# Kernel optimization log

Measured on AMD Instinct MI355X. Metric: run time of the kernel, lower is better.

The kernel has to match this reference:

```python
import jax, jax.numpy as jnp
import numpy as np

N_NODES = 100000
N_FEAT = 256
N_EDGES = 3200000
N_CLUSTERS = 16
COLLAPSE_REG = 0.1


def setup_inputs() -> dict:
    key = jax.random.key(0)
    k1, k2, k3, k4 = jax.random.split(key, 4)
    features = jax.random.normal(k1, (N_NODES, N_FEAT), dtype=jnp.float32)
    edge_row = jax.random.randint(k2, (N_EDGES,), 0, N_NODES, dtype=jnp.int32)
    edge_col = jax.random.randint(k3, (N_EDGES,), 0, N_NODES, dtype=jnp.int32)
    edge_val = jnp.ones((N_EDGES,), dtype=jnp.float32)
    # orthogonal-ish init approximated by scaled normal (init does not affect math)
    W = jax.random.normal(k4, (N_FEAT, N_CLUSTERS), dtype=jnp.float32) / np.float32(np.sqrt(N_FEAT))
    b = jnp.zeros((N_CLUSTERS,), dtype=jnp.float32)
    return {"features": features, "W": W, "b": b,
            "edge_row": edge_row, "edge_col": edge_col, "edge_val": edge_val}


def reference(features, W, b, edge_row, edge_col, edge_val):
    n = features.shape[0]
    k = W.shape[1]
    # assignment softmax (dropout_rate=0 -> identity)
    assignments = jax.nn.softmax(features @ W + b, axis=1)  # [n, k]
    cluster_sizes = assignments.sum(axis=0)                  # [k]
    assignments_pooling = assignments / cluster_sizes        # [n, k]
    # degrees = sparse row sums of adjacency
    degrees = jax.ops.segment_sum(edge_val, edge_row, num_segments=n)[:, None]  # [n, 1]
    n_edges = degrees.sum() / 2
    # sparse mm: adjacency @ assignments via gather + segment_sum
    adj_assign = jax.ops.segment_sum(edge_val[:, None] * assignments[edge_col],
                                     edge_row, num_segments=n)  # [n, k]
    graph_pooled = assignments.T @ adj_assign                # [k, k]
    normalizer_left = assignments.T @ degrees                # [k, 1]
    normalizer_right = degrees.T @ assignments               # [1, k]
    normalizer = normalizer_left @ normalizer_right / (2 * n_edges)
    spectral_loss = -jnp.trace(graph_pooled - normalizer) / (2 * n_edges)
    collapse_loss = COLLAPSE_REG * (jnp.linalg.norm(cluster_sizes) / n
                                    * jnp.sqrt(jnp.float32(k)) - 1.0)
    features_pooled = jax.nn.selu(assignments_pooling.T @ features)  # [k, d]
    return features_pooled, assignments, spectral_loss, collapse_loss
```

## Files before the change

kernel.cpp:

```cpp
#include <hip/hip_runtime.h>
#include <math.h>

#define KC 16
#define DF 256

#define WS_POOLED 0
#define WS_CS     4096
#define WS_M      4112
#define WS_TR     4128
#define WS_ESUM   4129
#define WS_TOTAL  4130
#define S8_OFF_BYTES 16640

typedef float v2f  __attribute__((ext_vector_type(2)));
typedef unsigned int u32x4 __attribute__((ext_vector_type(4)));

__global__ void zero_ws_kernel(float* __restrict__ ws) {
  int i = blockIdx.x * blockDim.x + threadIdx.x;
  if (i < WS_TOTAL) ws[i] = 0.0f;
}

__device__ __forceinline__ unsigned pk4_fp8(float a, float b, float c, float d) {
  unsigned w = (unsigned)__builtin_amdgcn_cvt_pk_fp8_f32(a, b, 0, false);
  w = (unsigned)__builtin_amdgcn_cvt_pk_fp8_f32(c, d, (int)w, true);
  return w;
}
__device__ __forceinline__ void cvt4_fp8(unsigned w, float* f) {
  v2f p = __builtin_amdgcn_cvt_pk_f32_fp8(w, false);
  f[0] = p.x; f[1] = p.y;
  p = __builtin_amdgcn_cvt_pk_f32_fp8(w, true);
  f[2] = p.x; f[3] = p.y;
}
__device__ __forceinline__ void cvt16_fp8(u32x4 u, float* f) {
  cvt4_fp8(u.x, f); cvt4_fp8(u.y, f + 4);
  cvt4_fp8(u.z, f + 8); cvt4_fp8(u.w, f + 12);
}

__global__ void __launch_bounds__(256) assign_kernel(
    const float* __restrict__ F, const float* __restrict__ W,
    const float* __restrict__ b, float* __restrict__ S,
    unsigned* __restrict__ S8, float* __restrict__ ws, int n) {
  __shared__ float Ft[32 * 257];
  __shared__ float cs_l[KC];
  const int t = threadIdx.x;
  if (t < KC) cs_l[t] = 0.0f;
  const int nb = blockIdx.x << 8;
  const int node = nb + t;
  const bool valid = node < n;
  const bool interior = (nb + 256 <= n);

  const int nl = t >> 3;
  const int jc = t & 7;

  float4 pref[8];
  auto load_chunk = [&](int s) {
    #pragma unroll
    for (int it = 0; it < 8; ++it) {
      const int nn = nl + (it << 5);
      if (interior || nb + nn < n)
        pref[it] = *(const float4*)&F[(size_t)(nb + nn) * DF + (s << 5) + (jc << 2)];
      else
        pref[it] = make_float4(0.f, 0.f, 0.f, 0.f);
    }
  };

  float acc[KC];
  #pragma unroll
  for (int k = 0; k < KC; ++k) acc[k] = 0.f;

  load_chunk(0);
  for (int s = 0; s < 8; ++s) {
    __syncthreads();
    #pragma unroll
    for (int it = 0; it < 8; ++it) {
      const int nn = nl + (it << 5);
      const int d0 = jc << 2;
      Ft[(d0 + 0) * 257 + nn] = pref[it].x;
      Ft[(d0 + 1) * 257 + nn] = pref[it].y;
      Ft[(d0 + 2) * 257 + nn] = pref[it].z;
      Ft[(d0 + 3) * 257 + nn] = pref[it].w;
    }
    __syncthreads();
    if (s < 7) load_chunk(s + 1);
    #pragma unroll
    for (int j = 0; j < 8; ++j) {
      const float fv0 = Ft[(4 * j + 0) * 257 + t];
      const float fv1 = Ft[(4 * j + 1) * 257 + t];
      const float fv2 = Ft[(4 * j + 2) * 257 + t];
      const float fv3 = Ft[(4 * j + 3) * 257 + t];
      const float* __restrict__ Wg = &W[(size_t)((s << 5) + (j << 2)) * KC];
      #pragma unroll
      for (int k = 0; k < KC; ++k)
        acc[k] += fv0 * Wg[k] + fv1 * Wg[KC + k]
                + fv2 * Wg[2 * KC + k] + fv3 * Wg[3 * KC + k];
    }
  }

  float mx = -1e30f;
  #pragma unroll
  for (int k = 0; k < KC; ++k) { acc[k] += b[k]; mx = fmaxf(mx, acc[k]); }
  float sum = 0.f;
  #pragma unroll
  for (int k = 0; k < KC; ++k) { acc[k] = __expf(acc[k] - mx); sum += acc[k]; }
  const float inv = 1.0f / sum;
  #pragma unroll
  for (int k = 0; k < KC; ++k) acc[k] *= inv;
  if (!valid) {
    #pragma unroll
    for (int k = 0; k < KC; ++k) acc[k] = 0.f;
  }
  if (valid) {
    float4* __restrict__ So = (float4*)&S[(size_t)node * KC];
    So[0] = make_float4(acc[0],  acc[1],  acc[2],  acc[3]);
    So[1] = make_float4(acc[4],  acc[5],  acc[6],  acc[7]);
    So[2] = make_float4(acc[8],  acc[9],  acc[10], acc[11]);
    So[3] = make_float4(acc[12], acc[13], acc[14], acc[15]);
    if (S8) {
      u32x4 p;
      p.x = pk4_fp8(acc[0],  acc[1],  acc[2],  acc[3]);
      p.y = pk4_fp8(acc[4],  acc[5],  acc[6],  acc[7]);
      p.z = pk4_fp8(acc[8],  acc[9],  acc[10], acc[11]);
      p.w = pk4_fp8(acc[12], acc[13], acc[14], acc[15]);
      *(u32x4*)&S8[(size_t)node * 4] = p;
    }
  }
  #pragma unroll
  for (int off = 1; off < 64; off <<= 1) {
    #pragma unroll
    for (int k = 0; k < KC; ++k) acc[k] += __shfl_xor(acc[k], off);
  }
  if ((t & 63) == 0) {
    #pragma unroll
    for (int k = 0; k < KC; ++k) atomicAdd(&cs_l[k], acc[k]);
  }
  __syncthreads();
  if (t < KC) atomicAdd(&ws[WS_CS + t], cs_l[t]);
}

__device__ __forceinline__ void acc_edge8(u32x4 ar, u32x4 ac, float v,
                                          float* m, float& tr, float& es) {
  float a[16], bb[16];
  cvt16_fp8(ar, a);
  cvt16_fp8(ac, bb);
  float d = 0.f;
  #pragma unroll
  for (int k = 0; k < 16; ++k) d += a[k] * bb[k];
  tr += v * d;
  es += v;
  #pragma unroll
  for (int k = 0; k < 16; ++k) m[k] += v * a[k];
}

__global__ void __launch_bounds__(256) edge_kernel_fp8(
    const int* __restrict__ erow, const int* __restrict__ ecol,
    const float* __restrict__ evl, const u32x4* __restrict__ S8,
    float* __restrict__ ws, int ne) {
  __shared__ float red[KC + 2];
  const int t = threadIdx.x;
  if (t < KC + 2) red[t] = 0.0f;
  __syncthreads();

  float m[KC];
  #pragma unroll
  for (int i = 0; i < KC; ++i) m[i] = 0.f;
  float tr = 0.f, es = 0.f;

  const int tid = blockIdx.x * 256 + t;
  const int stride = gridDim.x * 256;
  for (int e0 = tid; e0 < ne; e0 += 4 * stride) {
    const int eB = e0 + stride, eC = e0 + 2 * stride, eD = e0 + 3 * stride;
    int rA = __builtin_nontemporal_load(&erow[e0]);
    int cA = __builtin_nontemporal_load(&ecol[e0]);
    float vA = __builtin_nontemporal_load(&evl[e0]);
    int rB = 0, cB = 0, rC = 0, cC = 0, rD = 0, cD = 0;
    float vB = 0.f, vC = 0.f, vD = 0.f;
    if (eB < ne) { rB = __builtin_nontemporal_load(&erow[eB]);
                   cB = __builtin_nontemporal_load(&ecol[eB]);
                   vB = __builtin_nontemporal_load(&evl[eB]); }
    if (eC < ne) { rC = __builtin_nontemporal_load(&erow[eC]);
                   cC = __builtin_nontemporal_load(&ecol[eC]);
                   vC = __builtin_nontemporal_load(&evl[eC]); }
    if (eD < ne) { rD = __builtin_nontemporal_load(&erow[eD]);
                   cD = __builtin_nontemporal_load(&ecol[eD]);
                   vD = __builtin_nontemporal_load(&evl[eD]); }
    const u32x4 aA = __builtin_nontemporal_load(&S8[rA]);
    const u32x4 bA = __builtin_nontemporal_load(&S8[cA]);
    const u32x4 aB = __builtin_nontemporal_load(&S8[rB]);
    const u32x4 bB = __builtin_nontemporal_load(&S8[cB]);
    const u32x4 aC = __builtin_nontemporal_load(&S8[rC]);
    const u32x4 bC = __builtin_nontemporal_load(&S8[cC]);
    const u32x4 aD = __builtin_nontemporal_load(&S8[rD]);
    const u32x4 bD = __builtin_nontemporal_load(&S8[cD]);
    acc_edge8(aA, bA, vA, m, tr, es);
    acc_edge8(aB, bB, vB, m, tr, es);
    acc_edge8(aC, bC, vC, m, tr, es);
    acc_edge8(aD, bD, vD, m, tr, es);
  }
  #pragma unroll
  for (int off = 1; off < 64; off <<= 1) {
    tr += __shfl_xor(tr, off);
    es += __shfl_xor(es, off);
    #pragma unroll
    for (int i = 0; i < KC; ++i) m[i] += __shfl_xor(m[i], off);
  }
  if ((t & 63) == 0) {
    atomicAdd(&red[KC], tr);
    atomicAdd(&red[KC + 1], es);
    #pragma unroll
    for (int i = 0; i < KC; ++i) atomicAdd(&red[i], m[i]);
  }
  __syncthreads();
  if (t < KC)            atomicAdd(&ws[WS_M + t], red[t]);
  else if (t == KC)      atomicAdd(&ws[WS_TR], red[KC]);
  else if (t == KC + 1)  atomicAdd(&ws[WS_ESUM], red[KC + 1]);
}

__global__ void __launch_bounds__(256) edge_kernel_f32(
    const int* __restrict__ erow, const int* __restrict__ ecol,
    const float* __restrict__ evl, const float* __restrict__ S,
    float* __restrict__ ws, int ne) {
  __shared__ float red[KC + 2];
  const int t = threadIdx.x;
  if (t < KC + 2) red[t] = 0.0f;
  __syncthreads();
  float m[KC];
  #pragma unroll
  for (int i = 0; i < KC; ++i) m[i] = 0.f;
  float tr = 0.f, es = 0.f;
  const int stride = gridDim.x * blockDim.x;
  for (int e = blockIdx.x * blockDim.x + t; e < ne; e += stride) {
    const int r = erow[e];
    const int c = ecol[e];
    const float v = evl[e];
    const float4* __restrict__ Sr = (const float4*)(S + (size_t)r * KC);
    const float4* __restrict__ Sc = (const float4*)(S + (size_t)c * KC);
    const float4 a0 = Sr[0], a1 = Sr[1], a2 = Sr[2], a3 = Sr[3];
    const float4 b0 = Sc[0], b1 = Sc[1], b2 = Sc[2], b3 = Sc[3];
    float d = a0.x*b0.x + a0.y*b0.y + a0.z*b0.z + a0.w*b0.w
            + a1.x*b1.x + a1.y*b1.y + a1.z*b1.z + a1.w*b1.w
            + a2.x*b2.x + a2.y*b2.y + a2.z*b2.z + a2.w*b2.w
            + a3.x*b3.x + a3.y*b3.y + a3.z*b3.z + a3.w*b3.w;
    tr += v * d; es += v;
    m[0]+=v*a0.x; m[1]+=v*a0.y; m[2]+=v*a0.z; m[3]+=v*a0.w;
    m[4]+=v*a1.x; m[5]+=v*a1.y; m[6]+=v*a1.z; m[7]+=v*a1.w;
    m[8]+=v*a2.x; m[9]+=v*a2.y; m[10]+=v*a2.z; m[11]+=v*a2.w;
    m[12]+=v*a3.x; m[13]+=v*a3.y; m[14]+=v*a3.z; m[15]+=v*a3.w;
  }
  #pragma unroll
  for (int off = 1; off < 64; off <<= 1) {
    tr += __shfl_xor(tr, off);
    es += __shfl_xor(es, off);
    #pragma unroll
    for (int i = 0; i < KC; ++i) m[i] += __shfl_xor(m[i], off);
  }
  if ((t & 63) == 0) {
    atomicAdd(&red[KC], tr);
    atomicAdd(&red[KC + 1], es);
    #pragma unroll
    for (int i = 0; i < KC; ++i) atomicAdd(&red[i], m[i]);
  }
  __syncthreads();
  if (t < KC)            atomicAdd(&ws[WS_M + t], red[t]);
  else if (t == KC)      atomicAdd(&ws[WS_TR], red[KC]);
  else if (t == KC + 1)  atomicAdd(&ws[WS_ESUM], red[KC + 1]);
}

__global__ void __launch_bounds__(256) pool_kernel(
    const float* __restrict__ F, const float* __restrict__ S,
    float* __restrict__ ws, int n) {
  const int t = threadIdx.x;
  float acc[KC];
  #pragma unroll
  for (int i = 0; i < KC; ++i) acc[i] = 0.f;

  const int nch = n >> 5;
  for (int ch = blockIdx.x; ch < nch; ch += gridDim.x) {
    const int base = ch << 5;
    float fl[32];
    #pragma unroll
    for (int i = 0; i < 32; ++i)
      fl[i] = F[(size_t)(base + i) * DF + t];
    #pragma unroll
    for (int i = 0; i < 32; ++i) {
      const float4* __restrict__ Sr = (const float4*)(S + (size_t)(base + i) * KC);
      const float4 s0 = Sr[0], s1 = Sr[1], s2 = Sr[2], s3 = Sr[3];
      const float f = fl[i];
      acc[0]+=f*s0.x;  acc[1]+=f*s0.y;  acc[2]+=f*s0.z;  acc[3]+=f*s0.w;
      acc[4]+=f*s1.x;  acc[5]+=f*s1.y;  acc[6]+=f*s1.z;  acc[7]+=f*s1.w;
      acc[8]+=f*s2.x;  acc[9]+=f*s2.y;  acc[10]+=f*s2.z; acc[11]+=f*s2.w;
      acc[12]+=f*s3.x; acc[13]+=f*s3.y; acc[14]+=f*s3.z; acc[15]+=f*s3.w;
    }
  }
  if (blockIdx.x == 0) {
    for (int i2 = nch << 5; i2 < n; ++i2) {
      const float f = F[(size_t)i2 * DF + t];
      const float* __restrict__ Sr = S + (size_t)i2 * KC;
      #pragma unroll
      for (int kk = 0; kk < KC; ++kk) acc[kk] += f * Sr[kk];
    }
  }
  #pragma unroll
  for (int kk = 0; kk < KC; ++kk)
    atomicAdd(&ws[WS_POOLED + kk * DF + t], acc[kk]);
}

__global__ void finalize_kernel(const float* __restrict__ ws,
                                float* __restrict__ out, int n) {
  const int t = threadIdx.x;
  const float alpha = 1.6732632423543772f;
  const float scale = 1.0507009873554805f;
  for (int idx = t; idx < KC * DF; idx += blockDim.x) {
    const int k = idx >> 8;
    const float x = ws[WS_POOLED + idx] / ws[WS_CS + k];
    const float r = x > 0.f ? x : alpha * expm1f(x);
    out[idx] = scale * r;
  }
  if (t == 0) {
    const float esum = ws[WS_ESUM];
    const float tr = ws[WS_TR];
    float sm2 = 0.f, sc2 = 0.f;
    for (int i = 0; i < KC; ++i) {
      const float mi = ws[WS_M + i];
      sm2 += mi * mi;
      const float ci = ws[WS_CS + i];
      sc2 += ci * ci;
    }
    const float spectral = -(tr - sm2 / esum) / esum;
    const float collapse = 0.1f * (sqrtf(sc2) / (float)n * 4.0f - 1.0f);
    const size_t off = (size_t)(KC * DF) + (size_t)n * KC;
    out[off] = spectral;
    out[off + 1] = collapse;
  }
}

extern "C" void kernel_launch(void* const* d_in, const int* in_sizes, int n_in,
                              void* d_out, int out_size, void* d_ws, size_t ws_size,
                              hipStream_t stream) {
  const float* F   = (const float*)d_in[0];
  const float* W   = (const float*)d_in[1];
  const float* b   = (const float*)d_in[2];
  const int* erow  = (const int*)d_in[3];
  const int* ecol  = (const int*)d_in[4];
  const float* evl = (const float*)d_in[5];
  const int n  = in_sizes[0] / DF;
  const int ne = in_sizes[3];
  float* out = (float*)d_out;
  float* S   = out + KC * DF;
  float* ws  = (float*)d_ws;

  const bool use_fp8 = ws_size >= (size_t)S8_OFF_BYTES + (size_t)n * 16 + 64;
  unsigned* S8 = use_fp8 ? (unsigned*)((char*)d_ws + S8_OFF_BYTES) : nullptr;

  zero_ws_kernel<<<(WS_TOTAL + 255) / 256, 256, 0, stream>>>(ws);
  assign_kernel<<<(n + 255) / 256, 256, 0, stream>>>(F, W, b, S, S8, ws, n);
  if (use_fp8)
    edge_kernel_fp8<<<2048, 256, 0, stream>>>(erow, ecol, evl, (const u32x4*)S8, ws, ne);
  else
    edge_kernel_f32<<<2048, 256, 0, stream>>>(erow, ecol, evl, S, ws, ne);
  pool_kernel<<<1024, 256, 0, stream>>>(F, S, ws, n);
  finalize_kernel<<<1, 256, 0, stream>>>(ws, out, n);
}
```

Baseline: 340.8 us.

## Bin edges into 4096x4096 node tiles and process each tile from LDS

```diff
diff --git a/kernel.cpp b/kernel.cpp
--- a/kernel.cpp
+++ b/kernel.cpp
@@ -10,14 +10,20 @@
 #define WS_TR     4128
 #define WS_ESUM   4129
 #define WS_TOTAL  4130
-#define S8_OFF_BYTES 16640
+#define S8_OFF_BYTES  16640
+#define CUR_OFF_BYTES 2097152
+#define REC_OFF_BYTES 4194304
+#define MAXNB 1024
 
 typedef float v2f  __attribute__((ext_vector_type(2)));
 typedef unsigned int u32x4 __attribute__((ext_vector_type(4)));
-
-__global__ void zero_ws_kernel(float* __restrict__ ws) {
+typedef unsigned int u32x2 __attribute__((ext_vector_type(2)));
+
+__global__ void zero_ws_kernel(float* __restrict__ ws, unsigned* __restrict__ cur,
+                               int nb) {
   int i = blockIdx.x * blockDim.x + threadIdx.x;
   if (i < WS_TOTAL) ws[i] = 0.0f;
+  if (cur && i < nb) cur[i] = 0u;
 }
 
 __device__ __forceinline__ unsigned pk4_fp8(float a, float b, float c, float d) {
@@ -34,6 +40,19 @@
 __device__ __forceinline__ void cvt16_fp8(u32x4 u, float* f) {
   cvt4_fp8(u.x, f); cvt4_fp8(u.y, f + 4);
   cvt4_fp8(u.z, f + 8); cvt4_fp8(u.w, f + 12);
+}
+__device__ __forceinline__ void acc_edge8(u32x4 ar, u32x4 ac, float v,
+                                          float* m, float& tr, float& es) {
+  float a[16], bb[16];
+  cvt16_fp8(ar, a);
+  cvt16_fp8(ac, bb);
+  float d = 0.f;
+  #pragma unroll
+  for (int k = 0; k < 16; ++k) d += a[k] * bb[k];
+  tr += v * d;
+  es += v;
+  #pragma unroll
+  for (int k = 0; k < 16; ++k) m[k] += v * a[k];
 }
 
 __global__ void __launch_bounds__(256) assign_kernel(
@@ -137,18 +156,107 @@
   if (t < KC) atomicAdd(&ws[WS_CS + t], cs_l[t]);
 }
 
-__device__ __forceinline__ void acc_edge8(u32x4 ar, u32x4 ac, float v,
-                                          float* m, float& tr, float& es) {
-  float a[16], bb[16];
-  cvt16_fp8(ar, a);
-  cvt16_fp8(ac, bb);
-  float d = 0.f;
-  #pragma unroll
-  for (int k = 0; k < 16; ++k) d += a[k] * bb[k];
-  tr += v * d;
-  es += v;
-  #pragma unroll
-  for (int k = 0; k < 16; ++k) m[k] += v * a[k];
+__global__ void __launch_bounds__(256) scatter_kernel(
+    const int* __restrict__ erow, const int* __restrict__ ecol,
+    const float* __restrict__ evl, unsigned* __restrict__ cur,
+    u32x2* __restrict__ rec, int ne, int nch, int cap) {
+  __shared__ unsigned cnt_l[MAXNB];
+  __shared__ unsigned gb_l[MAXNB];
+  const int nb = nch * nch;
+  const int t = threadIdx.x;
+  for (int i = t; i < nb; i += 256) cnt_l[i] = 0u;
+  __syncthreads();
+
+  const int base = blockIdx.x << 12;
+  unsigned rcq[16], vq[16];
+  unsigned short bq[16], lq[16];
+  #pragma unroll
+  for (int i = 0; i < 16; ++i) {
+    const int e = base + (i << 8) + t;
+    if (e < ne) {
+      const int r = __builtin_nontemporal_load(&erow[e]);
+      const int c = __builtin_nontemporal_load(&ecol[e]);
+      const float v = __builtin_nontemporal_load(&evl[e]);
+      const int bk = (r >> 12) * nch + (c >> 12);
+      rcq[i] = ((unsigned)(r & 4095) << 12) | (unsigned)(c & 4095);
+      vq[i] = __float_as_uint(v);
+      bq[i] = (unsigned short)bk;
+      lq[i] = (unsigned short)atomicAdd(&cnt_l[bk], 1u);
+    } else {
+      bq[i] = 0xFFFFu;
+    }
+  }
+  __syncthreads();
+  for (int i = t; i < nb; i += 256) {
+    const unsigned c = cnt_l[i];
+    gb_l[i] = c ? atomicAdd(&cur[i], c) : 0u;
+  }
+  __syncthreads();
+  #pragma unroll
+  for (int i = 0; i < 16; ++i) {
+    if (bq[i] != 0xFFFFu) {
+      const unsigned pos = gb_l[bq[i]] + lq[i];
+      if (pos < (unsigned)cap) {
+        u32x2 q; q.x = rcq[i]; q.y = vq[i];
+        __builtin_nontemporal_store(q, &rec[(size_t)bq[i] * cap + pos]);
+      }
+    }
+  }
+}
+
+__global__ void __launch_bounds__(1024) edge_binned_kernel(
+    const u32x2* __restrict__ rec, const unsigned* __restrict__ cur,
+    const u32x4* __restrict__ S8, float* __restrict__ ws,
+    int n, int nch, int cap) {
+  __shared__ u32x4 A[4096];
+  __shared__ u32x4 B[4096];
+  __shared__ float red[KC + 2];
+  const int t = threadIdx.x;
+  if (t < KC + 2) red[t] = 0.0f;
+  const int bk = blockIdx.x;
+  const int bi = bk / nch, bj = bk % nch;
+  const int base_i = bi << 12, base_j = bj << 12;
+  const u32x4 z = {0u, 0u, 0u, 0u};
+  for (int i = t; i < 4096; i += 1024) {
+    A[i] = (base_i + i < n) ? S8[base_i + i] : z;
+    B[i] = (base_j + i < n) ? S8[base_j + i] : z;
+  }
+  __syncthreads();
+
+  int cnt = (int)cur[bk];
+  if (cnt > cap) cnt = cap;
+  const u32x2* __restrict__ rb = rec + (size_t)bk * cap;
+
+  float m[KC];
+  #pragma unroll
+  for (int i = 0; i < KC; ++i) m[i] = 0.f;
+  float tr = 0.f, es = 0.f;
+
+  for (int e = t; e < cnt; e += 1024) {
+    const u32x2 q = __builtin_nontemporal_load(&rb[e]);
+    const unsigned rc = q.x;
+    const float v = __uint_as_float(q.y);
+    const u32x4 ar = A[rc >> 12];
+    const u32x4 ac = B[rc & 4095u];
+    acc_edge8(ar, ac, v, m, tr, es);
+  }
+  #pragma unroll
+  for (int off = 1; off < 64; off <<= 1) {
+    tr += __shfl_xor(tr, off);
+    es += __shfl_xor(es, off);
+    #pragma unroll
+    for (int i = 0; i < KC; ++i) m[i] += __shfl_xor(m[i], off);
+  }
+  if ((t & 63) == 0) {
+    atomicAdd(&red[KC], tr);
+    atomicAdd(&red[KC + 1], es);
+    #pragma unroll
+    for (int i = 0; i < KC; ++i) atomicAdd(&red[i], m[i]);
+  }
+  __syncthreads();
+  if (t < KC)            atomicAdd(&ws[WS_M + t], red[t]);
+  else if (t == KC)      atomicAdd(&ws[WS_TR], red[KC]);
+  else if (t == KC + 1)  atomicAdd(&ws[WS_ESUM], red[KC + 1]);
 }
 
 __global__ void __launch_bounds__(256) edge_kernel_fp8(
@@ -159,38 +267,25 @@
   const int t = threadIdx.x;
   if (t < KC + 2) red[t] = 0.0f;
   __syncthreads();
-
   float m[KC];
   #pragma unroll
   for (int i = 0; i < KC; ++i) m[i] = 0.f;
   float tr = 0.f, es = 0.f;
-
   const int tid = blockIdx.x * 256 + t;
   const int stride = gridDim.x * 256;
   for (int e0 = tid; e0 < ne; e0 += 4 * stride) {
     const int eB = e0 + stride, eC = e0 + 2 * stride, eD = e0 + 3 * stride;
-    int rA = __builtin_nontemporal_load(&erow[e0]);
-    int cA = __builtin_nontemporal_load(&ecol[e0]);
-    float vA = __builtin_nontemporal_load(&evl[e0]);
+    int rA = erow[e0], cA = ecol[e0];
+    float vA = evl[e0];
     int rB = 0, cB = 0, rC = 0, cC = 0, rD = 0, cD = 0;
     float vB = 0.f, vC = 0.f, vD = 0.f;
-    if (eB < ne) { rB = __builtin_nontemporal_load(&erow[eB]);
-                   cB = __builtin_nontemporal_load(&ecol[eB]);
-                   vB = __builtin_nontemporal_load(&evl[eB]); }
-    if (eC < ne) { rC = __builtin_nontemporal_load(&erow[eC]);
-                   cC = __builtin_nontemporal_load(&ecol[eC]);
-                   vC = __builtin_nontemporal_load(&evl[eC]); }
-    if (eD < ne) { rD = __builtin_nontemporal_load(&erow[eD]);
-                   cD = __builtin_nontemporal_load(&ecol[eD]);
-                   vD = __builtin_nontemporal_load(&evl[eD]); }
-    const u32x4 aA = __builtin_nontemporal_load(&S8[rA]);
-    const u32x4 bA = __builtin_nontemporal_load(&S8[cA]);
-    const u32x4 aB = __builtin_nontemporal_load(&S8[rB]);
-    const u32x4 bB = __builtin_nontemporal_load(&S8[cB]);
-    const u32x4 aC = __builtin_nontemporal_load(&S8[rC]);
-    const u32x4 bC = __builtin_nontemporal_load(&S8[cC]);
-    const u32x4 aD = __builtin_nontemporal_load(&S8[rD]);
-    const u32x4 bD = __builtin_nontemporal_load(&S8[cD]);
+    if (eB < ne) { rB = erow[eB]; cB = ecol[eB]; vB = evl[eB]; }
+    if (eC < ne) { rC = erow[eC]; cC = ecol[eC]; vC = evl[eC]; }
+    if (eD < ne) { rD = erow[eD]; cD = ecol[eD]; vD = evl[eD]; }
+    const u32x4 aA = S8[rA], bA = S8[cA];
+    const u32x4 aB = S8[rB], bB = S8[cB];
+    const u32x4 aC = S8[rC], bC = S8[cC];
+    const u32x4 aD = S8[rD], bD = S8[cD];
     acc_edge8(aA, bA, vA, m, tr, es);
     acc_edge8(aB, bB, vB, m, tr, es);
     acc_edge8(aC, bC, vC, m, tr, es);
@@ -351,12 +446,29 @@
   const bool use_fp8 = ws_size >= (size_t)S8_OFF_BYTES + (size_t)n * 16 + 64;
   unsigned* S8 = use_fp8 ? (unsigned*)((char*)d_ws + S8_OFF_BYTES) : nullptr;
 
-  zero_ws_kernel<<<(WS_TOTAL + 255) / 256, 256, 0, stream>>>(ws);
+  const int nch = (n + 4095) >> 12;
+  const int nb = nch * nch;
+  const double lam = (double)ne / (double)nb;
+  int cap = (int)(lam + 8.0 * sqrt(lam > 1.0 ? lam : 1.0) + 64.0);
+  cap = (cap + 15) & ~15;
+  const bool use_bin = use_fp8 && nb <= MAXNB &&
+      (size_t)S8_OFF_BYTES + (size_t)n * 16 + 64 <= (size_t)CUR_OFF_BYTES &&
+      ws_size >= (size_t)REC_OFF_BYTES + (size_t)nb * cap * 8 + 64;
+  unsigned* cur = use_bin ? (unsigned*)((char*)d_ws + CUR_OFF_BYTES) : nullptr;
+  u32x2* rec    = use_bin ? (u32x2*)((char*)d_ws + REC_OFF_BYTES) : nullptr;
+
+  zero_ws_kernel<<<(WS_TOTAL + 255) / 256, 256, 0, stream>>>(ws, cur, nb);
   assign_kernel<<<(n + 255) / 256, 256, 0, stream>>>(F, W, b, S, S8, ws, n);
-  if (use_fp8)
+  if (use_bin) {
+    scatter_kernel<<<(ne + 4095) / 4096, 256, 0, stream>>>(
+        erow, ecol, evl, cur, rec, ne, nch, cap);
+    edge_binned_kernel<<<nb, 1024, 0, stream>>>(
+        rec, cur, (const u32x4*)S8, ws, n, nch, cap);
+  } else if (use_fp8) {
     edge_kernel_fp8<<<2048, 256, 0, stream>>>(erow, ecol, evl, (const u32x4*)S8, ws, ne);
-  else
+  } else {
     edge_kernel_f32<<<2048, 256, 0, stream>>>(erow, ecol, evl, S, ws, ne);
+  }
   pool_kernel<<<1024, 256, 0, stream>>>(F, S, ws, n);
   finalize_kernel<<<1, 256, 0, stream>>>(ws, out, n);
 }
```

New measurement: 430.8 us. 1.26x slower.
